# Performance work log

Hardware: AMD Instinct MI355X
Metric: run time of the kernel (lower is better)

## Reference

```python
import jax, jax.numpy as jnp
import numpy as np

D_MODEL, D_STATE, D_CONV, EXPAND = 1024, 16, 4, 2
D_INNER = EXPAND * D_MODEL            # 2048
DT_RANK = int(np.ceil(D_MODEL / 16))  # 64
B, L = 2, 2048


def _dt_bias(key):
    # matches torch init: dt ~ exp(U(log dt_min, log dt_max)), inv via softplus inverse
    dt = jnp.exp(jax.random.uniform(key, (D_INNER,)) * (np.log(0.1) - np.log(0.001)) + np.log(0.001))
    dt = jnp.clip(dt, 1e-4, None)
    return dt + jnp.log(-jnp.expm1(-dt))


def _A_log():
    return jnp.log(jnp.tile(jnp.arange(1, D_STATE + 1, dtype=jnp.float32)[None, :], (D_INNER, 1)))


def setup_inputs() -> dict:
    key = jax.random.key(0)
    ks = jax.random.split(key, 16)
    n = lambda k, shape, s=0.02: jax.random.normal(k, shape, jnp.float32) * s
    return {
        "hidden_states": jax.random.normal(ks[0], (B, L, D_MODEL), jnp.float32),
        "in_proj_w": n(ks[1], (2 * D_INNER, D_MODEL)),
        "conv_w": n(ks[2], (D_INNER, 1, D_CONV), 0.2),
        "conv_b": jnp.zeros((D_INNER,), jnp.float32),
        "x_proj_w": n(ks[3], (DT_RANK + 2 * D_STATE, D_INNER)),
        "dt_proj_w": n(ks[4], (D_INNER, DT_RANK), 0.1),
        "dt_proj_b": _dt_bias(ks[5]),
        "A_log": _A_log(),
        "D": jnp.ones((D_INNER,), jnp.float32),
        "conv_w_b": n(ks[6], (D_INNER, 1, D_CONV), 0.2),
        "conv_b_b": jnp.zeros((D_INNER,), jnp.float32),
        "x_proj_w_b": n(ks[7], (DT_RANK + 2 * D_STATE, D_INNER)),
        "dt_proj_w_b": n(ks[8], (D_INNER, DT_RANK), 0.1),
        "dt_proj_b_b": _dt_bias(ks[9]),
        "A_b_log": _A_log(),
        "D_b": jnp.ones((D_INNER,), jnp.float32),
        "out_proj_w": n(ks[10], (D_MODEL, D_INNER)),
    }


def _silu(x):
    return x * jax.nn.sigmoid(x)


def _causal_dw_conv(x, w, b):
    # x: (B, Di, L); w: (Di, 1, K) depthwise; left-pad K-1 => causal, output length L
    y = jax.lax.conv_general_dilated(
        x, w, window_strides=(1,), padding=[(D_CONV - 1, 0)],
        dimension_numbers=("NCH", "OIH", "NCH"), feature_group_count=x.shape[1])
    return y + b[None, :, None]


def _mamba_branch(xz, conv_w, conv_b, x_proj_w, dt_proj_w, dt_proj_b, A_log, Dp):
    # xz: (B, 2*Di, L) -> y: (B, Di, L); selective scan (mamba_inner_fn_no_out_proj)
    x, z = jnp.split(xz, 2, axis=1)
    x = _silu(_causal_dw_conv(x, conv_w, conv_b))                       # (B,Di,L)
    x_dbl = jnp.einsum('rd,bdl->brl', x_proj_w, x)
    dt_r, Bc, Cc = jnp.split(x_dbl, [DT_RANK, DT_RANK + D_STATE], axis=1)
    delta = jax.nn.softplus(jnp.einsum('dr,brl->bdl', dt_proj_w, dt_r) + dt_proj_b[None, :, None])
    A = -jnp.exp(A_log)                                                 # (Di,N)

    def step(h, inp):
        d_t, u_t, b_t, c_t = inp   # (B,Di),(B,Di),(B,N),(B,N)
        h = h * jnp.exp(d_t[..., None] * A) + (d_t * u_t)[..., None] * b_t[:, None, :]
        return h, jnp.einsum('bdn,bn->bd', h, c_t)

    h0 = jnp.zeros((x.shape[0], D_INNER, D_STATE), x.dtype)
    xs = (jnp.moveaxis(delta, 2, 0), jnp.moveaxis(x, 2, 0),
          jnp.moveaxis(Bc, 2, 0), jnp.moveaxis(Cc, 2, 0))
    _, ys = jax.lax.scan(step, h0, xs)                                  # (L,B,Di)
    y = jnp.moveaxis(ys, 0, 2) + x * Dp[None, :, None]
    return y * _silu(z)


def reference(hidden_states, in_proj_w, conv_w, conv_b, x_proj_w, dt_proj_w, dt_proj_b,
              A_log, D, conv_w_b, conv_b_b, x_proj_w_b, dt_proj_w_b, dt_proj_b_b,
              A_b_log, D_b, out_proj_w):
    # bimamba_type == 'v2': forward scan + flipped backward scan, summed, then out_proj (no biases)
    xz = jnp.einsum('ed,bld->bel', in_proj_w, hidden_states)            # (B, 2*Di, L)
    out_f = _mamba_branch(xz, conv_w, conv_b, x_proj_w, dt_proj_w, dt_proj_b, A_log, D)
    out_r = _mamba_branch(xz[..., ::-1], conv_w_b, conv_b_b, x_proj_w_b,
                          dt_proj_w_b, dt_proj_b_b, A_b_log, D_b)[..., ::-1]
    y = out_f + out_r                                                   # (B,Di,L)
    return jnp.einsum('me,bel->blm', out_proj_w, y)                     # (B,L,D)
```

## Files before the change

### kernel.cpp

```cpp
#include <hip/hip_runtime.h>
#include <hip/hip_bf16.h>
#include <math.h>


#define L_SEQ  2048
#define B_SZ   2
#define DM     1024
#define DI     2048
#define NST    16
#define RTOT   96
#define DTR    64
#define NTOT   (B_SZ * L_SEQ)
#define ETOT   (2 * DI)
#define SPLK   8
#define CHTMAX 64

#define LOG2E  1.44269504088896340736f

#define OFF_X    ((size_t)0)
#define OFF_ZT   (OFF_X   + (size_t)DI * NTOT)
#define OFF_XCF  (OFF_ZT  + (size_t)DI * NTOT)
#define OFF_XCB  (OFF_XCF + (size_t)DI * NTOT)
#define OFF_DLTB (OFF_XCB + (size_t)DI * NTOT)
#define OFF_XDF  (OFF_DLTB + (size_t)DI * NTOT)
#define OFF_XDB  (OFF_XDF + (size_t)RTOT * NTOT)
#define OFF_SS   (OFF_XDB + (size_t)RTOT * NTOT)
#define OFF_HL   (OFF_SS  + (size_t)4 * 32 * DI)
#define OFF_YGTF (OFF_HL  + (size_t)4 * 32 * NST * DI)
#define OFF_YGTB (OFF_YGTF + (size_t)NTOT * DI / 2)
#define OFF_XDT16F (OFF_YGTB + (size_t)NTOT * DI / 2)
#define OFF_XDT16B (OFF_XDT16F + (size_t)NTOT * DTR / 2)
#define OFF_DTW16F (OFF_XDT16B + (size_t)NTOT * DTR / 2)
#define OFF_DTW16B (OFF_DTW16F + (size_t)DI * DTR / 2)
#define WS_FLOATS  (OFF_DTW16B + (size_t)DI * DTR / 2)
#define WS64_FLOATS (WS_FLOATS + (size_t)4 * 64 * DI + (size_t)4 * 64 * NST * DI)

typedef __bf16 bf16x8 __attribute__((ext_vector_type(8)));
typedef float  floatx4 __attribute__((ext_vector_type(4)));

__device__ __forceinline__ float silu_f(float x) {
    return x / (1.f + __expf(-x));
}

__device__ __forceinline__ void gl2lds16(const __bf16* g, __bf16* l) {
    __builtin_amdgcn_global_load_lds(
        (const __attribute__((address_space(1))) unsigned int*)g,
        (__attribute__((address_space(3))) unsigned int*)l, 16, 0, 0);
}

template<int MT, bool TRANS, bool SPLITZ>
__global__ __launch_bounds__(256)
void gemm_bf16(const __bf16* __restrict__ A, const __bf16* __restrict__ B,
               float* __restrict__ C, float* __restrict__ C2,
               int M, int N, int K)
{
    static_assert(MT == 64 || MT == 128, "vmcnt literals assume MT in {64,128}");
    __shared__ __attribute__((aligned(16))) __bf16 As[2][MT * 32];
    __shared__ __attribute__((aligned(16))) __bf16 Bs[2][128 * 32];
    const int tid  = threadIdx.x;
    const int m0   = blockIdx.y * MT;
    const int n0   = blockIdx.x * 128;
    const int lane = tid & 63;
    const int wave = tid >> 6;
    const int wy   = wave >> 1, wx = wave & 1;
    const int lr   = lane & 15;
    const int q    = lane >> 4;
    constexpr int MF = MT / 32;

    floatx4 acc[MF][4];
#pragma unroll
    for (int i = 0; i < MF; ++i)
#pragma unroll
        for (int j = 0; j < 4; ++j) acc[i][j] = (floatx4)(0.0f);

    const int rl = lane >> 2;
    const int cp = lane & 3;
    const int sw = (q ^ ((lr >> 2) & 3)) * 8;

    auto stage = [&](int s, int k0) {
#pragma unroll
        for (int is = 0; is < MT / 64; ++is) {
            int r0  = wave * (MT / 4) + is * 16;
            int row = r0 + rl;
            int c   = cp ^ ((row >> 2) & 3);
            gl2lds16(A + (size_t)(m0 + row) * K + k0 + c * 8, &As[s][r0 * 32]);
        }
#pragma unroll
        for (int is = 0; is < 2; ++is) {
            int r0  = wave * 32 + is * 16;
            int row = r0 + rl;
            int c   = cp ^ ((row >> 2) & 3);
            gl2lds16(B + (size_t)(n0 + row) * K + k0 + c * 8, &Bs[s][r0 * 32]);
        }
    };

    stage(0, 0);
    int cur = 0;
    for (int k0 = 0; k0 < K; k0 += 32) {
        if (k0 + 32 < K) {
            stage(cur ^ 1, k0 + 32);
            if constexpr (MT == 128) {
                asm volatile("s_waitcnt vmcnt(4)" ::: "memory");
            } else {
                asm volatile("s_waitcnt vmcnt(3)" ::: "memory");
            }
        } else {
            asm volatile("s_waitcnt vmcnt(0)" ::: "memory");
        }
        __builtin_amdgcn_s_barrier();

        bf16x8 af[MF], bfr[4];
#pragma unroll
        for (int i = 0; i < MF; ++i)
            af[i] = *(const bf16x8*)&As[cur][(wy * (MT / 2) + i * 16 + lr) * 32 + sw];
#pragma unroll
        for (int j = 0; j < 4; ++j)
            bfr[j] = *(const bf16x8*)&Bs[cur][(wx * 64 + j * 16 + lr) * 32 + sw];
#pragma unroll
        for (int i = 0; i < MF; ++i)
#pragma unroll
            for (int j = 0; j < 4; ++j)
                acc[i][j] = __builtin_amdgcn_mfma_f32_16x16x32_bf16(
                    af[i], bfr[j], acc[i][j], 0, 0, 0);
        __builtin_amdgcn_s_barrier();
        cur ^= 1;
    }

    const int mb = m0 + wy * (MT / 2);
    const int nb = n0 + wx * 64;
#pragma unroll
    for (int i = 0; i < MF; ++i) {
#pragma unroll
        for (int j = 0; j < 4; ++j) {
            int gn  = nb + j * 16 + lr;
            int gm0 = mb + i * 16 + q * 4;
            if constexpr (SPLITZ) {
                if (m0 < DI) {
#pragma unroll
                    for (int r = 0; r < 4; ++r)
                        C[(size_t)(gm0 + r) * N + gn] = acc[i][j][r];
                } else {
                    *(floatx4*)&C2[(size_t)gn * DI + (gm0 - DI)] = acc[i][j];
                }
            } else if constexpr (TRANS) {
                *(floatx4*)&C[(size_t)gn * M + gm0] = acc[i][j];
            } else {
#pragma unroll
                for (int r = 0; r < 4; ++r)
                    C[(size_t)(gm0 + r) * N + gn] = acc[i][j][r];
            }
        }
    }
}

__global__ __launch_bounds__(256)
void dtproj_mfma(const __bf16* __restrict__ Af, const __bf16* __restrict__ Ab,
                 const __bf16* __restrict__ Bwf, const __bf16* __restrict__ Bwb,
                 const float* __restrict__ bif, const float* __restrict__ bib,
                 float* __restrict__ outf, float* __restrict__ outb)
{
    __shared__ __attribute__((aligned(16))) __bf16 As[2][128 * 32];
    __shared__ __attribute__((aligned(16))) __bf16 Bs[2][128 * 32];
    const int br = blockIdx.z;
    const __bf16* A  = br ? Ab : Af;
    const __bf16* B  = br ? Bwb : Bwf;
    const float*  bi = br ? bib : bif;
    float*        C  = br ? outb : outf;

    const int tid  = threadIdx.x;
    const int m0   = blockIdx.y * 128;
    const int n0   = blockIdx.x * 128;
    const int lane = tid & 63;
    const int wave = tid >> 6;
    const int wy   = wave >> 1, wx = wave & 1;
    const int lr   = lane & 15;
    const int q    = lane >> 4;

    floatx4 acc[4][4];
#pragma unroll
    for (int i = 0; i < 4; ++i)
#pragma unroll
        for (int j = 0; j < 4; ++j) acc[i][j] = (floatx4)(0.0f);

    const int rl = lane >> 2;
    const int cp = lane & 3;
    const int sw = (q ^ ((lr >> 2) & 3)) * 8;

#pragma unroll
    for (int t = 0; t < 2; ++t) {
        int k0 = t * 32;
#pragma unroll
        for (int is = 0; is < 2; ++is) {
            int r0  = wave * 32 + is * 16;
            int row = r0 + rl;
            int c   = cp ^ ((row >> 2) & 3);
            gl2lds16(A + (size_t)(m0 + row) * DTR + k0 + c * 8, &As[t][r0 * 32]);
            gl2lds16(B + (size_t)(n0 + row) * DTR + k0 + c * 8, &Bs[t][r0 * 32]);
        }
    }

#pragma unroll
    for (int t = 0; t < 2; ++t) {
        if (t == 0) asm volatile("s_waitcnt vmcnt(4)" ::: "memory");
        else        asm volatile("s_waitcnt vmcnt(0)" ::: "memory");
        __builtin_amdgcn_s_barrier();

        bf16x8 af[4], bfr[4];
#pragma unroll
        for (int i = 0; i < 4; ++i)
            af[i] = *(const bf16x8*)&As[t][(wy * 64 + i * 16 + lr) * 32 + sw];
#pragma unroll
        for (int j = 0; j < 4; ++j)
            bfr[j] = *(const bf16x8*)&Bs[t][(wx * 64 + j * 16 + lr) * 32 + sw];
#pragma unroll
        for (int i = 0; i < 4; ++i)
#pragma unroll
            for (int j = 0; j < 4; ++j)
                acc[i][j] = __builtin_amdgcn_mfma_f32_16x16x32_bf16(
                    af[i], bfr[j], acc[i][j], 0, 0, 0);
    }

    const int mb = m0 + wy * 64;
    const int nb = n0 + wx * 64;
    float bj[4];
#pragma unroll
    for (int j = 0; j < 4; ++j) bj[j] = bi[nb + j * 16 + lr];
#pragma unroll
    for (int i = 0; i < 4; ++i) {
#pragma unroll
        for (int r = 0; r < 4; ++r) {
            int gm = mb + i * 16 + q * 4 + r;
#pragma unroll
            for (int j = 0; j < 4; ++j) {
                int gn = nb + j * 16 + lr;
                float x = acc[i][j][r] + bj[j];
                float o = (x > 20.f) ? x : __logf(1.f + __expf(x));
                C[(size_t)gm * DI + gn] = o;
            }
        }
    }
}

__global__ __launch_bounds__(256)
void cvt2_bf16_k(const float* __restrict__ ia, __bf16* __restrict__ oa,
                 const float* __restrict__ ib, __bf16* __restrict__ ob)
{
    const float* in  = blockIdx.y ? ib : ia;
    __bf16*      out = blockIdx.y ? ob : oa;
    const size_t i = ((size_t)blockIdx.x * 256 + threadIdx.x) * 8;
    float4 a = *(const float4*)(in + i);
    float4 b = *(const float4*)(in + i + 4);
    bf16x8 p;
    p[0]=(__bf16)a.x; p[1]=(__bf16)a.y; p[2]=(__bf16)a.z; p[3]=(__bf16)a.w;
    p[4]=(__bf16)b.x; p[5]=(__bf16)b.y; p[6]=(__bf16)b.z; p[7]=(__bf16)b.w;
    *(bf16x8*)(out + i) = p;
}

__global__ __launch_bounds__(256)
void cvt_bf16_k(const float* __restrict__ in, __bf16* __restrict__ out)
{
    const size_t i = ((size_t)blockIdx.x * 256 + threadIdx.x) * 8;
    float4 a = *(const float4*)(in + i);
    float4 b = *(const float4*)(in + i + 4);
    bf16x8 p;
    p[0]=(__bf16)a.x; p[1]=(__bf16)a.y; p[2]=(__bf16)a.z; p[3]=(__bf16)a.w;
    p[4]=(__bf16)b.x; p[5]=(__bf16)b.y; p[6]=(__bf16)b.z; p[7]=(__bf16)b.w;
    *(bf16x8*)(out + i) = p;
}

__global__ __launch_bounds__(256)
void gatesum_k(const __bf16* __restrict__ a, const __bf16* __restrict__ b,
               const float* __restrict__ z, __bf16* __restrict__ o)
{
    const size_t i = ((size_t)blockIdx.x * 256 + threadIdx.x) * 8;
    bf16x8 x = *(const bf16x8*)(a + i);
    bf16x8 y = *(const bf16x8*)(b + i);
    float4 z0 = *(const float4*)(z + i);
    float4 z1 = *(const float4*)(z + i + 4);
    float zz[8] = { z0.x, z0.y, z0.z, z0.w, z1.x, z1.y, z1.z, z1.w };
    bf16x8 s;
#pragma unroll
    for (int e = 0; e < 8; ++e)
        s[e] = (__bf16)(((float)x[e] + (float)y[e]) * silu_f(zz[e]));
    *(bf16x8*)(o + i) = s;
}

__global__ __launch_bounds__(256)
void gemm_k3(const float* __restrict__ Af, const float* __restrict__ Bmf,
             float* __restrict__ Cf,
             const float* __restrict__ Ab, const float* __restrict__ Bmb,
             float* __restrict__ Cb,
             int M, int N, int K)
{
    __shared__ float As[16][132];
    __shared__ float Bs[16][132];
    const int tid = threadIdx.x;
    const int n0 = blockIdx.x * 128;
    const int m0 = blockIdx.y * 128;
    const int zz = blockIdx.z;
    const int brc = (zz >= SPLK) ? 1 : 0;
    const int kz  = zz & (SPLK - 1);
    const float* A  = brc ? Ab : Af;
    const float* Bm = brc ? Bmb : Bmf;
    float* C = (brc ? Cb : Cf) + (size_t)kz * M * N;
    int ksz  = K / SPLK;
    int kbeg = kz * ksz;
    int kend = kbeg + ksz;
    const int tx = tid & 15, ty = tid >> 4;

    float acc[8][8];
#pragma unroll
    for (int i = 0; i < 8; ++i)
#pragma unroll
        for (int j = 0; j < 8; ++j) acc[i][j] = 0.f;

    for (int k0 = kbeg; k0 < kend; k0 += 16) {
#pragma unroll
        for (int it = 0; it < 2; ++it) {
            int i = tid + it * 256;
            int m = i >> 2, kq = i & 3;
            float4 v = make_float4(0.f, 0.f, 0.f, 0.f);
            int gm = m0 + m;
            if (gm < M) v = *(const float4*)(A + (size_t)gm * K + (k0 + kq * 4));
            As[kq * 4 + 0][m] = v.x; As[kq * 4 + 1][m] = v.y;
            As[kq * 4 + 2][m] = v.z; As[kq * 4 + 3][m] = v.w;
        }
#pragma unroll
        for (int it = 0; it < 2; ++it) {
            int i = tid + it * 256;
            int n = i >> 2, kq = i & 3;
            float4 v = *(const float4*)(Bm + (size_t)(n0 + n) * K + (k0 + kq * 4));
            Bs[kq * 4 + 0][n] = v.x; Bs[kq * 4 + 1][n] = v.y;
            Bs[kq * 4 + 2][n] = v.z; Bs[kq * 4 + 3][n] = v.w;
        }
        __syncthreads();
#pragma unroll
        for (int kk = 0; kk < 16; ++kk) {
            float av[8], bv[8];
            *(float4*)&av[0] = *(const float4*)&As[kk][ty * 8];
            *(float4*)&av[4] = *(const float4*)&As[kk][ty * 8 + 4];
            *(float4*)&bv[0] = *(const float4*)&Bs[kk][tx * 8];
            *(float4*)&bv[4] = *(const float4*)&Bs[kk][tx * 8 + 4];
#pragma unroll
            for (int i = 0; i < 8; ++i)
#pragma unroll
                for (int j = 0; j < 8; ++j)
                    acc[i][j] = fmaf(av[i], bv[j], acc[i][j]);
        }
        __syncthreads();
    }

#pragma unroll
    for (int i = 0; i < 8; ++i) {
        int gm = m0 + ty * 8 + i;
        if (gm < M) {
            float* cp = C + (size_t)gm * N + n0 + tx * 8;
            *(float4*)cp       = make_float4(acc[i][0], acc[i][1], acc[i][2], acc[i][3]);
            *(float4*)(cp + 4) = make_float4(acc[i][4], acc[i][5], acc[i][6], acc[i][7]);
        }
    }
}

__global__ __launch_bounds__(256)
void reduce8t_k(const float* __restrict__ Pf, float* __restrict__ outf,
                __bf16* __restrict__ out2f,
                const float* __restrict__ Pb, float* __restrict__ outb,
                __bf16* __restrict__ out2b, size_t stride)
{
    const float* P   = blockIdx.y ? Pb : Pf;
    float*      outp = blockIdx.y ? outb : outf;
    __bf16*     out2 = blockIdx.y ? out2b : out2f;
    const size_t i4 = ((size_t)blockIdx.x * 256 + threadIdx.x) * 4;
    float4 s = *(const float4*)(P + i4);
#pragma unroll
    for (int z = 1; z < SPLK; ++z) {
        float4 v = *(const float4*)(P + (size_t)z * stride + i4);
        s.x += v.x; s.y += v.y; s.z += v.z; s.w += v.w;
    }
    *(float4*)(outp + i4) = s;
    const int r = (int)(i4 >> 12);
    if (r < DTR) {
        const int n = (int)(i4 & (NTOT - 1));
        out2[(size_t)(n + 0) * DTR + r] = (__bf16)s.x;
        out2[(size_t)(n + 1) * DTR + r] = (__bf16)s.y;
        out2[(size_t)(n + 2) * DTR + r] = (__bf16)s.z;
        out2[(size_t)(n + 3) * DTR + r] = (__bf16)s.w;
    }
}

__global__ __launch_bounds__(256)
void conv_k(const float* __restrict__ x,
            const float* __restrict__ wf, const float* __restrict__ bf,
            const float* __restrict__ wb, const float* __restrict__ bb,
            float* __restrict__ xcf, float* __restrict__ xcb)
{
    __shared__ float xs[70 * 65];
    const int tid = threadIdx.x;
    const int d0 = blockIdx.x * 64;
    const int n0 = blockIdx.y * 64;
    const int b  = n0 >> 11;
    const int l0 = n0 & (L_SEQ - 1);
    const size_t bbase = (size_t)b << 11;

    for (int i = tid; i < 64 * 70; i += 256) {
        int r = i / 70, c = i % 70;
        int l = l0 - 3 + c;
        float v = 0.f;
        if (l >= 0 && l < L_SEQ) v = x[(size_t)(d0 + r) * NTOT + bbase + l];
        xs[c * 65 + r] = v;
    }
    __syncthreads();

    const int dd = tid & 63;
    const int lq = tid >> 6;
    const int d  = d0 + dd;
    const float w0 = wf[d * 4 + 0], w1 = wf[d * 4 + 1];
    const float w2 = wf[d * 4 + 2], w3 = wf[d * 4 + 3];
    const float v0 = wb[d * 4 + 0], v1 = wb[d * 4 + 1];
    const float v2 = wb[d * 4 + 2], v3 = wb[d * 4 + 3];
    const float bfv = bf[d], bbv = bb[d];

    for (int lr = 0; lr < 64; lr += 4) {
        const int lo = lr + lq;
        const int l  = l0 + lo;
        float x0 = xs[(lo + 0) * 65 + dd];
        float x1 = xs[(lo + 1) * 65 + dd];
        float x2 = xs[(lo + 2) * 65 + dd];
        float x3 = xs[(lo + 3) * 65 + dd];
        float x4 = xs[(lo + 4) * 65 + dd];
        float x5 = xs[(lo + 5) * 65 + dd];
        float x6 = xs[(lo + 6) * 65 + dd];
        float xf = bfv + w0 * x0 + w1 * x1 + w2 * x2 + w3 * x3;
        xcf[((size_t)bbase + l) * DI + d] = silu_f(xf);
        float xb = bbv + v3 * x3 + v2 * x4 + v1 * x5 + v0 * x6;
        xcb[((size_t)bbase + (L_SEQ - 1 - l)) * DI + d] = silu_f(xb);
    }
}

__global__ __launch_bounds__(256)
void scan_part1(const float* __restrict__ xcf, const float* __restrict__ xcb,
                const float* __restrict__ xdf, const float* __restrict__ xdb,
                const float* __restrict__ dltf, const float* __restrict__ dltb,
                const float* __restrict__ Alog_f, const float* __restrict__ Alog_b,
                float* __restrict__ SS, float* __restrict__ HL,
                int nch, int csh)
{
    __shared__ float Bsh[NST][CHTMAX];
    const int cht = 1 << csh;
    const int tid = threadIdx.x;
    const int d  = blockIdx.x * 256 + tid;
    const int c  = blockIdx.y;
    const int bb = blockIdx.z;
    const int b  = bb & 1;
    const int br = bb >> 1;

    const float* u    = br ? xcb : xcf;
    const float* dl   = br ? dltb : dltf;
    const float* xd   = br ? xdb : xdf;
    const float* Alog = br ? Alog_b : Alog_f;

    const size_t nbase = (size_t)b * L_SEQ + (size_t)c * cht;
    const float* bcB = xd + (size_t)DTR * NTOT + nbase;

    for (int i = tid; i < NST * cht; i += 256) {
        int n = i >> csh;
        int t = i & (cht - 1);
        Bsh[n][t] = bcB[(size_t)n * NTOT + t];
    }

    float Arow[NST], h[NST];
#pragma unroll
    for (int n = 0; n < NST; ++n) {
        Arow[n] = -__expf(Alog[d * NST + n]) * LOG2E;
        h[n] = 0.f;
    }
    float S = 0.f;

    const float* up = u  + nbase * DI + d;
    const float* dp = dl + nbase * DI + d;

    __syncthreads();

    float dva[4], uva[4], dvb[4], uvb[4];
#pragma unroll
    for (int k = 0; k < 4; ++k) {
        dva[k] = dp[(size_t)k * DI];
        uva[k] = up[(size_t)k * DI];
    }
#pragma unroll
    for (int k = 0; k < 4; ++k) {
        dvb[k] = dp[(size_t)(4 + k) * DI];
        uvb[k] = up[(size_t)(4 + k) * DI];
    }

    for (int tr = 0; tr < cht; tr += 4) {
        float dvn[4], uvn[4];
#pragma unroll
        for (int k = 0; k < 4; ++k) {
            dvn[k] = dp[(size_t)(tr + 8 + k) * DI];
            uvn[k] = up[(size_t)(tr + 8 + k) * DI];
        }
        S += (dva[0] + dva[1]) + (dva[2] + dva[3]);
        float du[4] = { dva[0]*uva[0], dva[1]*uva[1], dva[2]*uva[2], dva[3]*uva[3] };
#pragma unroll
        for (int n = 0; n < NST; ++n) {
            float4 Bn = *(const float4*)&Bsh[n][tr];
            float hn = h[n];
            float An = Arow[n];
            hn = hn * __builtin_amdgcn_exp2f(dva[0] * An) + du[0] * Bn.x;
            hn = hn * __builtin_amdgcn_exp2f(dva[1] * An) + du[1] * Bn.y;
            hn = hn * __builtin_amdgcn_exp2f(dva[2] * An) + du[2] * Bn.z;
            hn = hn * __builtin_amdgcn_exp2f(dva[3] * An) + du[3] * Bn.w;
            h[n] = hn;
        }
#pragma unroll
        for (int k = 0; k < 4; ++k) {
            dva[k] = dvb[k]; uva[k] = uvb[k];
            dvb[k] = dvn[k]; uvb[k] = uvn[k];
        }
    }
    SS[((size_t)bb * nch + c) * DI + d] = S;
#pragma unroll
    for (int n = 0; n < NST; ++n)
        HL[(((size_t)bb * nch + c) * NST + n) * DI + d] = h[n];
}

__global__ __launch_bounds__(256)
void scan_part2(const float* __restrict__ SS, float* HL,
                const float* __restrict__ Alog_f, const float* __restrict__ Alog_b,
                int nch)
{
    const int d  = blockIdx.x * 256 + threadIdx.x;
    const int n  = blockIdx.y;
    const int bb = blockIdx.z;
    const int br = bb >> 1;
    const float* Alog = br ? Alog_b : Alog_f;
    const float A = -__expf(Alog[d * NST + n]) * LOG2E;

    float H = 0.f;
    for (int c = 0; c < nch; ++c) {
        const size_t si = ((size_t)bb * nch + c) * DI + d;
        const size_t hi = (((size_t)bb * nch + c) * NST + n) * DI + d;
        float hl = HL[hi];
        HL[hi] = H;
        H = __builtin_amdgcn_exp2f(SS[si] * A) * H + hl;
    }
}

__global__ __launch_bounds__(256)
void scan_part3(const float* __restrict__ xcf, const float* __restrict__ xcb,
                const float* __restrict__ xdf, const float* __restrict__ xdb,
                const float* __restrict__ dltf, const float* __restrict__ dltb,
                const float* __restrict__ HIN,
                __bf16* __restrict__ ygtf, __bf16* __restrict__ ygtb,
                const float* __restrict__ Alog_f, const float* __restrict__ Alog_b,
                const float* __restrict__ Df, const float* __restrict__ Db,
                int nch, int csh)
{
    __shared__ float BCs[2 * NST][CHTMAX];
    const int cht = 1 << csh;
    const int tid = threadIdx.x;
    const int d  = blockIdx.x * 256 + tid;
    const int c  = blockIdx.y;
    const int bb = blockIdx.z;
    const int b  = bb & 1;
    const int br = bb >> 1;

    const float* u    = br ? xcb : xcf;
    const float* dl   = br ? dltb : dltf;
    const float* xd   = br ? xdb : xdf;
    const float* Alog = br ? Alog_b : Alog_f;
    const float* Dv   = br ? Db : Df;
    __bf16*      ygt  = br ? ygtb : ygtf;

    const size_t nbase = (size_t)b * L_SEQ + (size_t)c * cht;
    const float* bcB = xd + (size_t)DTR * NTOT + nbase;

    for (int i = tid; i < 2 * NST * cht; i += 256) {
        int n = i >> csh;
        int t = i & (cht - 1);
        BCs[n][t] = bcB[(size_t)n * NTOT + t];
    }

    float Arow[NST], h[NST];
#pragma unroll
    for (int n = 0; n < NST; ++n) {
        Arow[n] = -__expf(Alog[d * NST + n]) * LOG2E;
        h[n] = HIN[(((size_t)bb * nch + c) * NST + n) * DI + d];
    }
    const float Dp = Dv[d];

    const float* up = u  + nbase * DI + d;
    const float* dp = dl + nbase * DI + d;
    const int    bL = b * L_SEQ;
    const int    t0 = c * cht;

    __syncthreads();

    float dva[4], uva[4], dvb[4], uvb[4];
#pragma unroll
    for (int k = 0; k < 4; ++k) {
        dva[k] = dp[(size_t)k * DI];
        uva[k] = up[(size_t)k * DI];
    }
#pragma unroll
    for (int k = 0; k < 4; ++k) {
        dvb[k] = dp[(size_t)(4 + k) * DI];
        uvb[k] = up[(size_t)(4 + k) * DI];
    }

    for (int tr = 0; tr < cht; tr += 4) {
        float dvn[4], uvn[4];
#pragma unroll
        for (int k = 0; k < 4; ++k) {
            dvn[k] = dp[(size_t)(tr + 8 + k) * DI];
            uvn[k] = up[(size_t)(tr + 8 + k) * DI];
        }

        float du[4] = { dva[0]*uva[0], dva[1]*uva[1], dva[2]*uva[2], dva[3]*uva[3] };
        float y[4] = { 0.f, 0.f, 0.f, 0.f };
#pragma unroll
        for (int n = 0; n < NST; ++n) {
            float4 Bn = *(const float4*)&BCs[n][tr];
            float4 Cn = *(const float4*)&BCs[NST + n][tr];
            float hn = h[n];
            float An = Arow[n];
            hn = hn * __builtin_amdgcn_exp2f(dva[0] * An) + du[0] * Bn.x;  y[0] = fmaf(hn, Cn.x, y[0]);
            hn = hn * __builtin_amdgcn_exp2f(dva[1] * An) + du[1] * Bn.y;  y[1] = fmaf(hn, Cn.y, y[1]);
            hn = hn * __builtin_amdgcn_exp2f(dva[2] * An) + du[2] * Bn.z;  y[2] = fmaf(hn, Cn.z, y[2]);
            hn = hn * __builtin_amdgcn_exp2f(dva[3] * An) + du[3] * Bn.w;  y[3] = fmaf(hn, Cn.w, y[3]);
            h[n] = hn;
        }
#pragma unroll
        for (int k = 0; k < 4; ++k) {
            int t = t0 + tr + k;
            int nn = br ? (bL + (L_SEQ - 1 - t)) : (bL + t);
            ygt[(size_t)nn * DI + d] = (__bf16)(y[k] + uva[k] * Dp);
        }
#pragma unroll
        for (int k = 0; k < 4; ++k) {
            dva[k] = dvb[k]; uva[k] = uvb[k];
            dvb[k] = dvn[k]; uvb[k] = uvn[k];
        }
    }
}

extern "C" void kernel_launch(void* const* d_in, const int* in_sizes, int n_in,
                              void* d_out, int out_size, void* d_ws, size_t ws_size,
                              hipStream_t stream)
{
    const float* hid     = (const float*)d_in[0];
    const float* inw     = (const float*)d_in[1];
    const float* convw   = (const float*)d_in[2];
    const float* convb   = (const float*)d_in[3];
    const float* xpw     = (const float*)d_in[4];
    const float* dtw     = (const float*)d_in[5];
    const float* dtb     = (const float*)d_in[6];
    const float* Alog    = (const float*)d_in[7];
    const float* Dv      = (const float*)d_in[8];
    const float* convw_b = (const float*)d_in[9];
    const float* convb_b = (const float*)d_in[10];
    const float* xpw_b   = (const float*)d_in[11];
    const float* dtw_b   = (const float*)d_in[12];
    const float* dtb_b   = (const float*)d_in[13];
    const float* Alog_b  = (const float*)d_in[14];
    const float* Dv_b    = (const float*)d_in[15];
    const float* outw    = (const float*)d_in[16];
    float* out = (float*)d_out;
    float* ws  = (float*)d_ws;

    if (ws_size < WS_FLOATS * sizeof(float)) return;

    const bool big = ws_size >= WS64_FLOATS * sizeof(float);
    const int  nch = big ? 64 : 32;
    const int  csh = big ? 5 : 6;

    float*  X    = ws + OFF_X;
    float*  ZT   = ws + OFF_ZT;
    float*  XCF  = ws + OFF_XCF;
    float*  XCB  = ws + OFF_XCB;
    float*  DLTB = ws + OFF_DLTB;
    float*  XDF  = ws + OFF_XDF;
    float*  XDB  = ws + OFF_XDB;
    float*  SS   = big ? (ws + WS_FLOATS) : (ws + OFF_SS);
    float*  HLb  = SS + (size_t)4 * nch * DI;
    __bf16* YGTF = (__bf16*)(ws + OFF_YGTF);
    __bf16* YGTB = (__bf16*)(ws + OFF_YGTB);
    float*  PF   = ws + OFF_YGTF;
    float*  PB   = ws + OFF_YGTB;
    float*  DLTF = X;
    __bf16* IW16 = (__bf16*)(ws + OFF_SS);
    __bf16* HD16 = IW16 + (size_t)ETOT * DM;
    __bf16* OW16 = (__bf16*)(ws + OFF_XCB);
    __bf16* YGS  = (__bf16*)(ws + OFF_XCF);
    __bf16* XDT16F = (__bf16*)(ws + OFF_XDT16F);
    __bf16* XDT16B = (__bf16*)(ws + OFF_XDT16B);
    __bf16* DTW16F = (__bf16*)(ws + OFF_DTW16F);
    __bf16* DTW16B = (__bf16*)(ws + OFF_DTW16B);

    dim3 blk(256);
    cvt2_bf16_k<<<dim3(ETOT * DM / 2048, 2), blk, 0, stream>>>(inw, IW16, hid, HD16);
    cvt2_bf16_k<<<dim3(DI * DTR / 2048, 2), blk, 0, stream>>>(dtw, DTW16F, dtw_b, DTW16B);
    gemm_bf16<128, false, true><<<dim3(32, 32), blk, 0, stream>>>(
        IW16, HD16, X, ZT, ETOT, NTOT, DM);
    conv_k<<<dim3(32, 64), blk, 0, stream>>>(X, convw, convb, convw_b, convb_b, XCF, XCB);
    gemm_k3<<<dim3(32, 1, 2 * SPLK), blk, 0, stream>>>(
        xpw, XCF, PF, xpw_b, XCB, PB, RTOT, NTOT, DI);
    reduce8t_k<<<dim3(RTOT * NTOT / 1024, 2), blk, 0, stream>>>(
        PF, XDF, XDT16F, PB, XDB, XDT16B, (size_t)RTOT * NTOT);
    dtproj_mfma<<<dim3(DI / 128, NTOT / 128, 2), blk, 0, stream>>>(
        XDT16F, XDT16B, DTW16F, DTW16B, dtb, dtb_b, DLTF, DLTB);
    scan_part1<<<dim3(DI / 256, nch, 4), blk, 0, stream>>>(
        XCF, XCB, XDF, XDB, DLTF, DLTB, Alog, Alog_b, SS, HLb, nch, csh);
    scan_part2<<<dim3(DI / 256, NST, 4), blk, 0, stream>>>(
        SS, HLb, Alog, Alog_b, nch);
    scan_part3<<<dim3(DI / 256, nch, 4), blk, 0, stream>>>(
        XCF, XCB, XDF, XDB, DLTF, DLTB, HLb, YGTF, YGTB, Alog, Alog_b, Dv, Dv_b,
        nch, csh);
    cvt_bf16_k<<<dim3(DM * DI / 2048), blk, 0, stream>>>(outw, OW16);
    gatesum_k<<<dim3(NTOT * DI / 2048), blk, 0, stream>>>(YGTF, YGTB, ZT, YGS);
    gemm_bf16<64, true, false><<<dim3(32, 16), blk, 0, stream>>>(
        OW16, YGS, out, nullptr, DM, NTOT, DI);

    (void)in_sizes; (void)n_in; (void)out_size;
}
```

Before: 437.3 us.

## Replace fp32 split-K x_proj GEMM and reduction with bf16 MFMA kernel

Computes the x_proj projection with a bf16 MFMA kernel that covers the full K dimension per block. This removes the fp32 SIMT split-K GEMM and its separate reduction pass. The conv kernel now also emits bf16 copies of its activations, and a small kernel converts and zero-pads the x_proj weights. The new GEMM launches only 64 blocks, so GPU occupancy is low, and bf16 inputs reduce the precision of the projection.

```diff
diff --git a/kernel.cpp b/kernel.cpp
--- a/kernel.cpp
+++ b/kernel.cpp
@@ -12,7 +12,6 @@
 #define DTR    64
 #define NTOT   (B_SZ * L_SEQ)
 #define ETOT   (2 * DI)
-#define SPLK   8
 #define CHTMAX 64
 
 #define LOG2E  1.44269504088896340736f
@@ -154,6 +153,101 @@
 }
 
 __global__ __launch_bounds__(256)
+void k3_mfma(const __bf16* __restrict__ Af, const __bf16* __restrict__ Ab,
+             const __bf16* __restrict__ Bf, const __bf16* __restrict__ Bb,
+             float* __restrict__ Cf, float* __restrict__ Cb,
+             __bf16* __restrict__ Tf, __bf16* __restrict__ Tb)
+{
+    __shared__ __attribute__((aligned(16))) __bf16 As[2][128 * 32];
+    __shared__ __attribute__((aligned(16))) __bf16 Bs[2][128 * 32];
+    const int br = blockIdx.z;
+    const __bf16* A = br ? Ab : Af;
+    const __bf16* B = br ? Bb : Bf;
+    float*        C = br ? Cb : Cf;
+    __bf16*       T = br ? Tb : Tf;
+
+    const int tid  = threadIdx.x;
+    const int n0   = blockIdx.x * 128;
+    const int lane = tid & 63;
+    const int wave = tid >> 6;
+    const int wy   = wave >> 1, wx = wave & 1;
+    const int lr   = lane & 15;
+    const int q    = lane >> 4;
+
+    floatx4 acc[4][4];
+#pragma unroll
+    for (int i = 0; i < 4; ++i)
+#pragma unroll
+        for (int j = 0; j < 4; ++j) acc[i][j] = (floatx4)(0.0f);
+
+    const int rl = lane >> 2;
+    const int cp = lane & 3;
+    const int sw = (q ^ ((lr >> 2) & 3)) * 8;
+
+    auto stage = [&](int s, int k0) {
+#pragma unroll
+        for (int is = 0; is < 2; ++is) {
+            int r0  = wave * 32 + is * 16;
+            int row = r0 + rl;
+            int c   = cp ^ ((row >> 2) & 3);
+            gl2lds16(A + (size_t)row * DI + k0 + c * 8, &As[s][r0 * 32]);
+        }
+#pragma unroll
+        for (int is = 0; is < 2; ++is) {
+            int r0  = wave * 32 + is * 16;
+            int row = r0 + rl;
+            int c   = cp ^ ((row >> 2) & 3);
+            gl2lds16(B + (size_t)(n0 + row) * DI + k0 + c * 8, &Bs[s][r0 * 32]);
+        }
+    };
+
+    stage(0, 0);
+    int cur = 0;
+    for (int k0 = 0; k0 < DI; k0 += 32) {
+        if (k0 + 32 < DI) {
+            stage(cur ^ 1, k0 + 32);
+            asm volatile("s_waitcnt vmcnt(4)" ::: "memory");
+        } else {
+            asm volatile("s_waitcnt vmcnt(0)" ::: "memory");
+        }
+        __builtin_amdgcn_s_barrier();
+
+        bf16x8 af[4], bfr[4];
+#pragma unroll
+        for (int i = 0; i < 4; ++i)
+            af[i] = *(const bf16x8*)&As[cur][(wy * 64 + i * 16 + lr) * 32 + sw];
+#pragma unroll
+        for (int j = 0; j < 4; ++j)
+            bfr[j] = *(const bf16x8*)&Bs[cur][(wx * 64 + j * 16 + lr) * 32 + sw];
+#pragma unroll
+        for (int i = 0; i < 4; ++i)
+#pragma unroll
+            for (int j = 0; j < 4; ++j)
+                acc[i][j] = __builtin_amdgcn_mfma_f32_16x16x32_bf16(
+                    af[i], bfr[j], acc[i][j], 0, 0, 0);
+        __builtin_amdgcn_s_barrier();
+        cur ^= 1;
+    }
+
+    const int mb = wy * 64;
+    const int nb = n0 + wx * 64;
+#pragma unroll
+    for (int i = 0; i < 4; ++i) {
+#pragma unroll
+        for (int j = 0; j < 4; ++j) {
+            int gn  = nb + j * 16 + lr;
+#pragma unroll
+            for (int r = 0; r < 4; ++r) {
+                int gm = mb + i * 16 + q * 4 + r;
+                float val = acc[i][j][r];
+                if (gm < RTOT) C[(size_t)gm * NTOT + gn] = val;
+                if (gm < DTR)  T[(size_t)gn * DTR + gm] = (__bf16)val;
+            }
+        }
+    }
+}
+
+__global__ __launch_bounds__(256)
 void dtproj_mfma(const __bf16* __restrict__ Af, const __bf16* __restrict__ Ab,
                  const __bf16* __restrict__ Bwf, const __bf16* __restrict__ Bwb,
                  const float* __restrict__ bif, const float* __restrict__ bib,
@@ -269,6 +363,27 @@
 }
 
 __global__ __launch_bounds__(256)
+void cvt_pad_xpw(const float* __restrict__ xf, const float* __restrict__ xb,
+                 __bf16* __restrict__ of, __bf16* __restrict__ ob)
+{
+    const float* in  = blockIdx.y ? xb : xf;
+    __bf16*      out = blockIdx.y ? ob : of;
+    const size_t i = ((size_t)blockIdx.x * 256 + threadIdx.x) * 8;
+    const int r = (int)(i / DI);
+    bf16x8 p;
+    if (r < RTOT) {
+        float4 a = *(const float4*)(in + i);
+        float4 b = *(const float4*)(in + i + 4);
+        p[0]=(__bf16)a.x; p[1]=(__bf16)a.y; p[2]=(__bf16)a.z; p[3]=(__bf16)a.w;
+        p[4]=(__bf16)b.x; p[5]=(__bf16)b.y; p[6]=(__bf16)b.z; p[7]=(__bf16)b.w;
+    } else {
+#pragma unroll
+        for (int e = 0; e < 8; ++e) p[e] = (__bf16)0.f;
+    }
+    *(bf16x8*)(out + i) = p;
+}
+
+__global__ __launch_bounds__(256)
 void gatesum_k(const __bf16* __restrict__ a, const __bf16* __restrict__ b,
                const float* __restrict__ z, __bf16* __restrict__ o)
 {
@@ -286,113 +401,11 @@
 }
 
 __global__ __launch_bounds__(256)
-void gemm_k3(const float* __restrict__ Af, const float* __restrict__ Bmf,
-             float* __restrict__ Cf,
-             const float* __restrict__ Ab, const float* __restrict__ Bmb,
-             float* __restrict__ Cb,
-             int M, int N, int K)
-{
-    __shared__ float As[16][132];
-    __shared__ float Bs[16][132];
-    const int tid = threadIdx.x;
-    const int n0 = blockIdx.x * 128;
-    const int m0 = blockIdx.y * 128;
-    const int zz = blockIdx.z;
-    const int brc = (zz >= SPLK) ? 1 : 0;
-    const int kz  = zz & (SPLK - 1);
-    const float* A  = brc ? Ab : Af;
-    const float* Bm = brc ? Bmb : Bmf;
-    float* C = (brc ? Cb : Cf) + (size_t)kz * M * N;
-    int ksz  = K / SPLK;
-    int kbeg = kz * ksz;
-    int kend = kbeg + ksz;
-    const int tx = tid & 15, ty = tid >> 4;
-
-    float acc[8][8];
-#pragma unroll
-    for (int i = 0; i < 8; ++i)
-#pragma unroll
-        for (int j = 0; j < 8; ++j) acc[i][j] = 0.f;
-
-    for (int k0 = kbeg; k0 < kend; k0 += 16) {
-#pragma unroll
-        for (int it = 0; it < 2; ++it) {
-            int i = tid + it * 256;
-            int m = i >> 2, kq = i & 3;
-            float4 v = make_float4(0.f, 0.f, 0.f, 0.f);
-            int gm = m0 + m;
-            if (gm < M) v = *(const float4*)(A + (size_t)gm * K + (k0 + kq * 4));
-            As[kq * 4 + 0][m] = v.x; As[kq * 4 + 1][m] = v.y;
-            As[kq * 4 + 2][m] = v.z; As[kq * 4 + 3][m] = v.w;
-        }
-#pragma unroll
-        for (int it = 0; it < 2; ++it) {
-            int i = tid + it * 256;
-            int n = i >> 2, kq = i & 3;
-            float4 v = *(const float4*)(Bm + (size_t)(n0 + n) * K + (k0 + kq * 4));
-            Bs[kq * 4 + 0][n] = v.x; Bs[kq * 4 + 1][n] = v.y;
-            Bs[kq * 4 + 2][n] = v.z; Bs[kq * 4 + 3][n] = v.w;
-        }
-        __syncthreads();
-#pragma unroll
-        for (int kk = 0; kk < 16; ++kk) {
-            float av[8], bv[8];
-            *(float4*)&av[0] = *(const float4*)&As[kk][ty * 8];
-            *(float4*)&av[4] = *(const float4*)&As[kk][ty * 8 + 4];
-            *(float4*)&bv[0] = *(const float4*)&Bs[kk][tx * 8];
-            *(float4*)&bv[4] = *(const float4*)&Bs[kk][tx * 8 + 4];
-#pragma unroll
-            for (int i = 0; i < 8; ++i)
-#pragma unroll
-                for (int j = 0; j < 8; ++j)
-                    acc[i][j] = fmaf(av[i], bv[j], acc[i][j]);
-        }
-        __syncthreads();
-    }
-
-#pragma unroll
-    for (int i = 0; i < 8; ++i) {
-        int gm = m0 + ty * 8 + i;
-        if (gm < M) {
-            float* cp = C + (size_t)gm * N + n0 + tx * 8;
-            *(float4*)cp       = make_float4(acc[i][0], acc[i][1], acc[i][2], acc[i][3]);
-            *(float4*)(cp + 4) = make_float4(acc[i][4], acc[i][5], acc[i][6], acc[i][7]);
-        }
-    }
-}
-
-__global__ __launch_bounds__(256)
-void reduce8t_k(const float* __restrict__ Pf, float* __restrict__ outf,
-                __bf16* __restrict__ out2f,
-                const float* __restrict__ Pb, float* __restrict__ outb,
-                __bf16* __restrict__ out2b, size_t stride)
-{
-    const float* P   = blockIdx.y ? Pb : Pf;
-    float*      outp = blockIdx.y ? outb : outf;
-    __bf16*     out2 = blockIdx.y ? out2b : out2f;
-    const size_t i4 = ((size_t)blockIdx.x * 256 + threadIdx.x) * 4;
-    float4 s = *(const float4*)(P + i4);
-#pragma unroll
-    for (int z = 1; z < SPLK; ++z) {
-        float4 v = *(const float4*)(P + (size_t)z * stride + i4);
-        s.x += v.x; s.y += v.y; s.z += v.z; s.w += v.w;
-    }
-    *(float4*)(outp + i4) = s;
-    const int r = (int)(i4 >> 12);
-    if (r < DTR) {
-        const int n = (int)(i4 & (NTOT - 1));
-        out2[(size_t)(n + 0) * DTR + r] = (__bf16)s.x;
-        out2[(size_t)(n + 1) * DTR + r] = (__bf16)s.y;
-        out2[(size_t)(n + 2) * DTR + r] = (__bf16)s.z;
-        out2[(size_t)(n + 3) * DTR + r] = (__bf16)s.w;
-    }
-}
-
-__global__ __launch_bounds__(256)
 void conv_k(const float* __restrict__ x,
             const float* __restrict__ wf, const float* __restrict__ bf,
             const float* __restrict__ wb, const float* __restrict__ bb,
-            float* __restrict__ xcf, float* __restrict__ xcb)
+            float* __restrict__ xcf, float* __restrict__ xcb,
+            __bf16* __restrict__ xc16f, __bf16* __restrict__ xc16b)
 {
     __shared__ float xs[70 * 65];
     const int tid = threadIdx.x;
@@ -431,9 +444,15 @@
         float x5 = xs[(lo + 5) * 65 + dd];
         float x6 = xs[(lo + 6) * 65 + dd];
         float xf = bfv + w0 * x0 + w1 * x1 + w2 * x2 + w3 * x3;
-        xcf[((size_t)bbase + l) * DI + d] = silu_f(xf);
+        float sf = silu_f(xf);
+        size_t nf = (size_t)bbase + l;
+        xcf[nf * DI + d]   = sf;
+        xc16f[nf * DI + d] = (__bf16)sf;
         float xb = bbv + v3 * x3 + v2 * x4 + v1 * x5 + v0 * x6;
-        xcb[((size_t)bbase + (L_SEQ - 1 - l)) * DI + d] = silu_f(xb);
+        float sb = silu_f(xb);
+        size_t nb2 = (size_t)bbase + (L_SEQ - 1 - l);
+        xcb[nb2 * DI + d]   = sb;
+        xc16b[nb2 * DI + d] = (__bf16)sb;
     }
 }
 
@@ -686,9 +705,11 @@
     float*  HLb  = SS + (size_t)4 * nch * DI;
     __bf16* YGTF = (__bf16*)(ws + OFF_YGTF);
     __bf16* YGTB = (__bf16*)(ws + OFF_YGTB);
-    float*  PF   = ws + OFF_YGTF;
-    float*  PB   = ws + OFF_YGTB;
+    __bf16* XC16F = (__bf16*)(ws + OFF_YGTF);
+    __bf16* XC16B = (__bf16*)(ws + OFF_YGTB);
     float*  DLTF = X;
+    __bf16* XPW16F = (__bf16*)(ws + OFF_X);
+    __bf16* XPW16B = XPW16F + (size_t)128 * DI;
     __bf16* IW16 = (__bf16*)(ws + OFF_SS);
     __bf16* HD16 = IW16 + (size_t)ETOT * DM;
     __bf16* OW16 = (__bf16*)(ws + OFF_XCB);
@@ -703,11 +724,12 @@
     cvt2_bf16_k<<<dim3(DI * DTR / 2048, 2), blk, 0, stream>>>(dtw, DTW16F, dtw_b, DTW16B);
     gemm_bf16<128, false, true><<<dim3(32, 32), blk, 0, stream>>>(
         IW16, HD16, X, ZT, ETOT, NTOT, DM);
-    conv_k<<<dim3(32, 64), blk, 0, stream>>>(X, convw, convb, convw_b, convb_b, XCF, XCB);
-    gemm_k3<<<dim3(32, 1, 2 * SPLK), blk, 0, stream>>>(
-        xpw, XCF, PF, xpw_b, XCB, PB, RTOT, NTOT, DI);
-    reduce8t_k<<<dim3(RTOT * NTOT / 1024, 2), blk, 0, stream>>>(
-        PF, XDF, XDT16F, PB, XDB, XDT16B, (size_t)RTOT * NTOT);
+    conv_k<<<dim3(32, 64), blk, 0, stream>>>(
+        X, convw, convb, convw_b, convb_b, XCF, XCB, XC16F, XC16B);
+    cvt_pad_xpw<<<dim3(128 * DI / 2048, 2), blk, 0, stream>>>(
+        xpw, xpw_b, XPW16F, XPW16B);
+    k3_mfma<<<dim3(32, 1, 2), blk, 0, stream>>>(
+        XPW16F, XPW16B, XC16F, XC16B, XDF, XDB, XDT16F, XDT16B);
     dtproj_mfma<<<dim3(DI / 128, NTOT / 128, 2), blk, 0, stream>>>(
         XDT16F, XDT16B, DTW16F, DTW16B, dtb, dtb_b, DLTF, DLTB);
     scan_part1<<<dim3(DI / 256, nch, 4), blk, 0, stream>>>(
```

Measured after the change: 426.7 us, median of 2. 2.4% less time.
